# Optimization experiments

Measured on AMD Instinct MI355X. Metric: run time of the kernel, lower is better.

Reference implementation:

```python
import jax, jax.numpy as jnp
import numpy as np

L, S, M, N, E, H = 1024, 1024, 256, 8, 512, 8


def embed_rotary(x, cos, sin):
    # x: [B, T, E]; interleaved rotate-half as in RotaryPositionEncoding.embed_rotary
    x2 = jnp.stack([-x[..., 1::2], x[..., 0::2]], axis=-1).reshape(x.shape)
    return x * cos + x2 * sin


def setup_inputs() -> dict:
    key = jax.random.key(0)
    ks = jax.random.split(key, 12)
    return {
        "query": jax.random.normal(ks[0], (L, N, E), jnp.float32),
        "key": jax.random.normal(ks[1], (S, N, E), jnp.float32),
        "value": jax.random.normal(ks[2], (S, N, E), jnp.float32),
        "in_proj_weight": jax.random.normal(ks[3], (3 * E, E), jnp.float32) / np.sqrt(E).astype(np.float32),
        "in_proj_bias": jnp.zeros((3 * E,), jnp.float32),
        "out_proj_weight": jax.random.normal(ks[4], (E, E), jnp.float32) / np.sqrt(E).astype(np.float32),
        "out_proj_bias": jnp.zeros((E,), jnp.float32),
        "rot_q": jax.random.normal(ks[5], (N, L, E, 2), jnp.float32),
        "rot_k": jax.random.normal(ks[6], (N, S, E, 2), jnp.float32),
        "k_mem": jax.random.normal(ks[7], (M, N, E), jnp.float32),
        "v_mem": jax.random.normal(ks[8], (M, N, E), jnp.float32),
        "gate_attn": jax.random.normal(ks[9], (H,), jnp.float32),
        "mem_mask": jax.random.randint(ks[10], (N, M), 0, 2).astype(bool),
        "num_heads": H,
    }


def reference(query, key, value, in_proj_weight, in_proj_bias, out_proj_weight,
              out_proj_bias, rot_q, rot_k, k_mem, v_mem, gate_attn, mem_mask, num_heads):
    L_, N_, E_ = query.shape
    S_ = key.shape[0]
    H_ = num_heads
    hd = E_ // H_
    scale = float(hd) ** -0.5
    # separate q/k/v projections (qkv not identical path)
    q = query @ in_proj_weight[:E_].T + in_proj_bias[:E_]
    k = key @ in_proj_weight[E_:2 * E_].T + in_proj_bias[E_:2 * E_]
    v = value @ in_proj_weight[2 * E_:].T + in_proj_bias[2 * E_:]
    q = q * scale
    # inline rotary PE (applied in batch-first layout, then back)
    q = embed_rotary(q.transpose(1, 0, 2), rot_q[..., 0], rot_q[..., 1]).transpose(1, 0, 2)
    k = embed_rotary(k.transpose(1, 0, 2), rot_k[..., 0], rot_k[..., 1]).transpose(1, 0, 2)
    qh = q.reshape(L_, N_, H_, hd).transpose(1, 2, 0, 3)  # [N,H,L,hd]
    kh = k.reshape(S_, N_, H_, hd).transpose(1, 2, 0, 3)  # [N,H,S,hd]
    vh = v.reshape(S_, N_, H_, hd).transpose(1, 2, 0, 3)
    scores = jnp.einsum('nhld,nhsd->nhls', qh, kh)
    # slot-competition: softmax over queries (slots), then renormalize over keys
    w = jax.nn.softmax(scores, axis=2) + 1e-8
    w = w / w.sum(axis=-1, keepdims=True)
    attn = jnp.einsum('nhls,nhsd->nhld', w, vh)
    # memorizing-transformer style memory K/V branch with sigmoid head gating
    Mm = k_mem.shape[0]
    km = k_mem.reshape(Mm, N_, H_, hd).transpose(1, 2, 0, 3)  # [N,H,M,hd]
    vm = v_mem.reshape(Mm, N_, H_, hd).transpose(1, 2, 0, 3)
    sm = jnp.einsum('nhld,nhmd->nhlm', qh, km)
    sm = jnp.where(mem_mask[:, None, None, :], -1e9, sm)  # additive -inf mask
    wm = jax.nn.softmax(sm, axis=-1)
    om = jnp.einsum('nhlm,nhmd->nhld', wm, vm)
    gate = jax.nn.sigmoid(gate_attn)[None, :, None, None]  # [1,H,1,1]
    attn = gate * om + (1.0 - gate) * attn
    out = attn.transpose(2, 0, 1, 3).reshape(L_, N_, E_)  # back to [L,N,E]
    return out @ out_proj_weight.T + out_proj_bias
```

## Files before the change

### kernel.cpp

```cpp
#include <hip/hip_runtime.h>
#include <hip/hip_bf16.h>

typedef __hip_bfloat16 bf16;
typedef __bf16 bf16x8 __attribute__((ext_vector_type(8)));
typedef float f32x4 __attribute__((ext_vector_type(4)));

#define LQ 1024
#define SK 1024
#define MMEM 256
#define NB 8
#define EE 512
#define NH 8
#define HD 64
#define NBH 64

__device__ inline __bf16 tobf(float f) {
  __hip_bfloat16 h = __float2bfloat16(f);
  return *reinterpret_cast<__bf16*>(&h);
}
__device__ inline float bf2f(__bf16 x) {
  unsigned short u; __builtin_memcpy(&u, &x, 2);
  unsigned int v = (unsigned int)u << 16;
  float f; __builtin_memcpy(&f, &v, 4);
  return f;
}
__device__ inline f32x4 MFMA(bf16x8 a, bf16x8 b, f32x4 c) {
  return __builtin_amdgcn_mfma_f32_16x16x32_bf16(a, b, c, 0, 0, 0);
}

__device__ inline void gload_lds16(const bf16* g, void* l) {
  __builtin_amdgcn_global_load_lds(
      (const __attribute__((address_space(1))) void*)g,
      (__attribute__((address_space(3))) void*)l, 16, 0, 0);
}

__device__ inline bf16x8 load8(const float* p) {
  float4 a = *(const float4*)p;
  float4 b = *(const float4*)(p + 4);
  bf16x8 r;
  r[0] = tobf(a.x); r[1] = tobf(a.y); r[2] = tobf(a.z); r[3] = tobf(a.w);
  r[4] = tobf(b.x); r[5] = tobf(b.y); r[6] = tobf(b.z); r[7] = tobf(b.w);
  return r;
}

#define CVT_T0 524288
#define CVT_T3 98304
#define CVT_T4 32768
__global__ __launch_bounds__(256) void convert5(
    const float* __restrict__ q, const float* __restrict__ k,
    const float* __restrict__ v, const float* __restrict__ w,
    const float* __restrict__ o, bf16* __restrict__ qc, bf16* __restrict__ kc,
    bf16* __restrict__ vc, bf16* __restrict__ wc, bf16* __restrict__ oc)
{
  long long t = (long long)blockIdx.x * 256 + threadIdx.x;
  const float* src; bf16* dst; long long idx;
  if (t < CVT_T0)               { src = q; dst = qc; idx = t; }
  else if (t < 2 * CVT_T0)      { src = k; dst = kc; idx = t - CVT_T0; }
  else if (t < 3 * CVT_T0)      { src = v; dst = vc; idx = t - 2 * CVT_T0; }
  else if (t < 3 * CVT_T0 + CVT_T3) { src = w; dst = wc; idx = t - 3 * CVT_T0; }
  else                          { src = o; dst = oc; idx = t - 3 * CVT_T0 - CVT_T3; }
  *(bf16x8*)(dst + idx * 8) = load8(src + idx * 8);
}

__global__ __launch_bounds__(256) void gemm_proj3(
    const bf16* __restrict__ qc, const bf16* __restrict__ kc,
    const bf16* __restrict__ vc, const bf16* __restrict__ ipwb,
    const float* __restrict__ ipb, bf16* __restrict__ pq,
    bf16* __restrict__ pk, bf16* __restrict__ v_raw)
{
  __shared__ __align__(16) char smem[33792];
  __bf16* As = (__bf16*)smem;
  __bf16* Bs = (__bf16*)(smem + 16384);
  const int z = blockIdx.z;
  const bf16* A = (z == 0) ? qc : (z == 1) ? kc : vc;
  const bf16* W = ipwb + (long long)z * EE * EE;
  const float* bias = ipb + z * EE;
  const float alpha = (z == 0) ? 0.125f : 1.f;
  const int bid2 = blockIdx.y * gridDim.x + blockIdx.x;
  const int xcd = bid2 & 7, sub = bid2 >> 3;
  const int by = (xcd << 3) + (sub >> 2);
  const int bx = sub & 3;
  const int tm0 = by << 7, tn0 = bx << 7;
  const int t = threadIdx.x;
  const int wave = t >> 6, lane = t & 63;
  const int wrow0 = (wave & 1) << 6, wcol0 = (wave >> 1) << 6;
  const int m16 = lane & 15, quad = lane >> 4;

  const f32x4 zero = {0.f, 0.f, 0.f, 0.f};
  f32x4 acc[4][4];
#pragma unroll
  for (int mi = 0; mi < 4; ++mi)
#pragma unroll
    for (int ni = 0; ni < 4; ++ni) acc[mi][ni] = zero;

  const bf16* Ab = A + (long long)tm0 * EE;
  const bf16* Bb = W + (long long)tn0 * EE;
  const int ob_u = wave << 10;

  for (int k0 = 0; k0 < EE; k0 += 64) {
#pragma unroll
    for (int c = 0; c < 4; ++c) {
      int ob = (c << 12) + ob_u;
      int obl = ob + (lane << 4);
      int row = obl >> 7;
      int ce = (obl & 127) >> 1;
      gload_lds16(Ab + (long long)row * EE + k0 + ce, smem + ob);
      gload_lds16(Bb + (long long)row * EE + k0 + ce, smem + 16384 + ob);
    }
    __syncthreads();
#pragma unroll
    for (int kh = 0; kh < 2; ++kh) {
      bf16x8 av[4], bv[4];
#pragma unroll
      for (int i = 0; i < 4; ++i) {
        av[i] = *(bf16x8*)(As + ((wrow0 + (i << 4) + m16) << 6) + (kh << 5) + (quad << 3));
        bv[i] = *(bf16x8*)(Bs + ((wcol0 + (i << 4) + m16) << 6) + (kh << 5) + (quad << 3));
      }
#pragma unroll
      for (int mi = 0; mi < 4; ++mi)
#pragma unroll
        for (int ni = 0; ni < 4; ++ni)
          acc[mi][ni] = MFMA(av[mi], bv[ni], acc[mi][ni]);
    }
    __syncthreads();
  }

  __bf16 (*Cs)[132] = (__bf16(*)[132])smem;
#pragma unroll
  for (int mi = 0; mi < 4; ++mi)
#pragma unroll
    for (int ni = 0; ni < 4; ++ni) {
      int col = wcol0 + (ni << 4) + m16;
      float bv = bias[tn0 + col];
#pragma unroll
      for (int r = 0; r < 4; ++r)
        Cs[wrow0 + (mi << 4) + (quad << 2) + r][col] =
            tobf((acc[mi][ni][r] + bv) * alpha);
    }
  __syncthreads();
  bf16* O = (z == 0) ? pq : (z == 1) ? pk : v_raw;
  const int crow = t >> 1, ch0 = (t & 1) << 6;
  long long gb = (long long)(tm0 + crow) * EE + tn0 + ch0;
#pragma unroll
  for (int j = 0; j < 64; j += 8)
    *(uint4*)(O + gb + j) = *(uint4*)&Cs[crow][ch0 + j];
}

__global__ __launch_bounds__(256) void rotary_kernel(
    const bf16* __restrict__ pq, const bf16* __restrict__ pk,
    const float* __restrict__ rot_q, const float* __restrict__ rot_k,
    bf16* __restrict__ Qh, bf16* __restrict__ Kh)
{
  const bf16* src = blockIdx.y ? pk : pq;
  const float* rot = blockIdx.y ? rot_k : rot_q;
  bf16* dst = blockIdx.y ? Kh : Qh;
  const int t = threadIdx.x;
  const int row = (blockIdx.x << 2) + (t >> 6);
  const int e0 = (t & 63) << 3;
  const int l = row >> 3, n = row & 7;
  bf16x8 x = *(const bf16x8*)(src + (long long)row * EE + e0);
  const float* rp = rot + ((((long long)n * LQ + l) * EE + e0) << 1);
  __bf16 vals[8];
#pragma unroll
  for (int j = 0; j < 8; j += 2) {
    float4 cs4 = *(const float4*)(rp + (j << 1));
    float x0 = bf2f(x[j]);
    float x1 = bf2f(x[j + 1]);
    vals[j]     = tobf(x0 * cs4.x - x1 * cs4.y);
    vals[j + 1] = tobf(x1 * cs4.z + x0 * cs4.w);
  }
  const int h = e0 >> 6, d0 = e0 & 63;
  *(uint4*)(dst + (((long long)(n * NH + h) * LQ + l) * HD + d0)) = *(uint4*)vals;
}

__global__ __launch_bounds__(256) void colsum_kernel(
    const bf16* __restrict__ Qh, const bf16* __restrict__ Kh,
    float* __restrict__ csum)
{
  __shared__ __align__(16) __bf16 Ks[64][72];
  __shared__ __align__(16) __bf16 Qs[64][72];
  __shared__ float cpart[64][2];
  const int bid = blockIdx.y * gridDim.x + blockIdx.x;
  const int xcd = bid & 7, sub = bid >> 3;
  const int b = (xcd << 3) + (sub >> 4);
  const int st0 = (sub & 15) << 6;
  const int t = threadIdx.x;
  const int lrow = t >> 2, lcol = (t & 3) << 4;
  const int wave = t >> 6, lane = t & 63;
  const int wm = (wave & 1) << 5, wn = (wave >> 1) << 5;
  const int m16 = lane & 15, quad = lane >> 4;

  {
    const bf16* kp = Kh + ((long long)b * SK + st0 + lrow) * HD + lcol;
    *(bf16x8*)&Ks[lrow][lcol] = *(const bf16x8*)kp;
    *(bf16x8*)&Ks[lrow][lcol + 8] = *(const bf16x8*)(kp + 8);
  }
  __syncthreads();
  bf16x8 bk[2][2];
#pragma unroll
  for (int ni = 0; ni < 2; ++ni)
#pragma unroll
    for (int kh = 0; kh < 2; ++kh)
      bk[ni][kh] = *(bf16x8*)&Ks[wn + (ni << 4) + m16][(kh << 5) + (quad << 3)];
  __syncthreads();

  const f32x4 zero = {0.f, 0.f, 0.f, 0.f};
  float colp[2] = {0.f, 0.f};
  const bf16* qbase = Qh + ((long long)b * LQ + lrow) * HD + lcol;
  bf16x8 qr0 = *(const bf16x8*)qbase;
  bf16x8 qr1 = *(const bf16x8*)(qbase + 8);
  for (int lt = 0; lt < 16; ++lt) {
    *(bf16x8*)&Qs[lrow][lcol] = qr0;
    *(bf16x8*)&Qs[lrow][lcol + 8] = qr1;
    __syncthreads();
    if (lt < 15) {
      const bf16* qp = qbase + (long long)((lt + 1) << 6) * HD;
      qr0 = *(const bf16x8*)qp;
      qr1 = *(const bf16x8*)(qp + 8);
    }
    f32x4 s00 = zero, s01 = zero, s10 = zero, s11 = zero;
#pragma unroll
    for (int kh = 0; kh < 2; ++kh) {
      bf16x8 a0 = *(bf16x8*)&Qs[wm + m16][(kh << 5) + (quad << 3)];
      bf16x8 a1 = *(bf16x8*)&Qs[wm + 16 + m16][(kh << 5) + (quad << 3)];
      s00 = MFMA(a0, bk[0][kh], s00);
      s01 = MFMA(a0, bk[1][kh], s01);
      s10 = MFMA(a1, bk[0][kh], s10);
      s11 = MFMA(a1, bk[1][kh], s11);
    }
    f32x4 sacc[2][2] = {{s00, s01}, {s10, s11}};
#pragma unroll
    for (int mi = 0; mi < 2; ++mi)
#pragma unroll
      for (int ni = 0; ni < 2; ++ni)
#pragma unroll
        for (int r = 0; r < 4; ++r)
          colp[ni] += __expf(sacc[mi][ni][r]);
    __syncthreads();
  }
  for (int ni = 0; ni < 2; ++ni) {
    float v = colp[ni];
    v += __shfl_down(v, 32, 64);
    v += __shfl_down(v, 16, 64);
    if (quad == 0) cpart[wn + (ni << 4) + m16][wm >> 5] = v;
  }
  __syncthreads();
  if (t < 64) csum[b * SK + st0 + t] = cpart[t][0] + cpart[t][1];
}

__global__ __launch_bounds__(256) void vsum_kernel(
    const bf16* __restrict__ Vt, float* __restrict__ Vsum)
{
  int wid = blockIdx.x * 4 + (threadIdx.x >> 6);
  int lane = threadIdx.x & 63;
  const bf16* p = Vt + (long long)wid * SK + lane * 16;
  float s = 0.f;
  bf16x8 v0 = *(const bf16x8*)p;
  bf16x8 v1 = *(const bf16x8*)(p + 8);
#pragma unroll
  for (int j = 0; j < 8; ++j) s += bf2f(v0[j]) + bf2f(v1[j]);
  for (int off = 32; off; off >>= 1) s += __shfl_down(s, off, 64);
  if (lane == 0) Vsum[wid] = s;
}

__global__ __launch_bounds__(256) void attn_fused(
    const bf16* __restrict__ Qh, const bf16* __restrict__ Kh,
    const bf16* __restrict__ Vt, const bf16* __restrict__ km,
    const bf16* __restrict__ vmt, const float* __restrict__ csum,
    const float* __restrict__ Vsum, const int* __restrict__ mask,
    const float* __restrict__ gate, bf16* __restrict__ comb)
{
  __shared__ __align__(16) __bf16 Ks[64][72];
  __shared__ __align__(16) __bf16 Vs[64][72];
  __shared__ __align__(16) __bf16 Ps[4096];
  __shared__ __align__(16) float rcs[SK];
  __shared__ __align__(16) float mskf[MMEM];
  __shared__ float rpa[64][2];
  __shared__ float rpm[64][2];
  const int bid = blockIdx.y * gridDim.x + blockIdx.x;
  const int xcd = bid & 7, sub = bid >> 3;
  const int b = (xcd << 3) + (sub >> 4);
  const int tm0 = (sub & 15) << 6;
  const int n = b >> 3, h = b & 7;
  const int t = threadIdx.x;
  const int lrow = t >> 2, lcol = (t & 3) << 4;
  const int wave = t >> 6, lane = t & 63;
  const int wm = (wave & 1) << 5, wn = (wave >> 1) << 5;
  const int m16 = lane & 15, quad = lane >> 4;
  const int swz = (m16 & 7) << 4;

#pragma unroll
  for (int i = 0; i < 4; ++i)
    rcs[t + i * 256] = 1.f / csum[b * SK + t + i * 256];
  mskf[t] = mask[n * MMEM + t] ? 0.f : 1.f;
  {
    const bf16* qp = Qh + ((long long)b * LQ + tm0 + lrow) * HD + lcol;
    *(bf16x8*)&Ks[lrow][lcol] = *(const bf16x8*)qp;
    *(bf16x8*)&Ks[lrow][lcol + 8] = *(const bf16x8*)(qp + 8);
  }
  __syncthreads();
  bf16x8 aq[2][2];
#pragma unroll
  for (int li = 0; li < 2; ++li)
#pragma unroll
    for (int kh = 0; kh < 2; ++kh)
      aq[li][kh] = *(bf16x8*)&Ks[wm + (li << 4) + m16][(kh << 5) + (quad << 3)];
  __syncthreads();

  const f32x4 zero = {0.f, 0.f, 0.f, 0.f};
  f32x4 m00 = zero, m01 = zero, m10 = zero, m11 = zero;
  float rsm[2] = {0.f, 0.f};
  {
    const bf16* kbase = km + ((long long)b * MMEM + lrow) * HD + lcol;
    const bf16* vbase = vmt + ((long long)b * HD + lrow) * MMEM + lcol;
    bf16x8 kr0 = *(const bf16x8*)kbase;
    bf16x8 kr1 = *(const bf16x8*)(kbase + 8);
    bf16x8 vr0 = *(const bf16x8*)vbase;
    bf16x8 vr1 = *(const bf16x8*)(vbase + 8);
    for (int mt = 0; mt < 4; ++mt) {
      *(bf16x8*)&Ks[lrow][lcol] = kr0;
      *(bf16x8*)&Ks[lrow][lcol + 8] = kr1;
      *(bf16x8*)&Vs[lrow][lcol] = vr0;
      *(bf16x8*)&Vs[lrow][lcol + 8] = vr1;
      __syncthreads();
      if (mt < 3) {
        const bf16* kp = kbase + (long long)((mt + 1) << 6) * HD;
        const bf16* vp = vbase + ((mt + 1) << 6);
        kr0 = *(const bf16x8*)kp;
        kr1 = *(const bf16x8*)(kp + 8);
        vr0 = *(const bf16x8*)vp;
        vr1 = *(const bf16x8*)(vp + 8);
      }
      f32x4 s00 = zero, s01 = zero, s10 = zero, s11 = zero;
      __builtin_amdgcn_s_setprio(1);
#pragma unroll
      for (int kh = 0; kh < 2; ++kh) {
        bf16x8 ak0 = *(bf16x8*)&Ks[wn + m16][(kh << 5) + (quad << 3)];
        bf16x8 ak1 = *(bf16x8*)&Ks[wn + 16 + m16][(kh << 5) + (quad << 3)];
        s00 = MFMA(ak0, aq[0][kh], s00);
        s01 = MFMA(ak0, aq[1][kh], s01);
        s10 = MFMA(ak1, aq[0][kh], s10);
        s11 = MFMA(ak1, aq[1][kh], s11);
      }
      __builtin_amdgcn_s_setprio(0);
      {
        char* pA = (char*)Ps + (wm + m16) * 128;
        char* pB = (char*)Ps + (wm + 16 + m16) * 128;
#pragma unroll
        for (int si = 0; si < 2; ++si) {
          int sloc = wn + (si << 4) + (quad << 2);
          f32x4 mf4 = *(const f32x4*)&mskf[(mt << 6) + sloc];
          f32x4 sA = si ? s10 : s00;
          f32x4 sB = si ? s11 : s01;
          __bf16 vA[4], vB[4];
#pragma unroll
          for (int r = 0; r < 4; ++r) {
            float pa = __expf(sA[r]) * mf4[r];
            rsm[0] += pa; vA[r] = tobf(pa);
            float pb = __expf(sB[r]) * mf4[r];
            rsm[1] += pb; vB[r] = tobf(pb);
          }
          int sbyte = (sloc << 1) ^ swz;
          *(uint2*)(pA + sbyte) = *(uint2*)vA;
          *(uint2*)(pB + sbyte) = *(uint2*)vB;
        }
      }
      __syncthreads();
      __builtin_amdgcn_s_setprio(1);
#pragma unroll
      for (int kh = 0; kh < 2; ++kh) {
        int sb = (kh << 6) + (quad << 4);
        bf16x8 ap0 = *(bf16x8*)((char*)Ps + (wm + m16) * 128 + (sb ^ swz));
        bf16x8 ap1 = *(bf16x8*)((char*)Ps + (wm + 16 + m16) * 128 + (sb ^ swz));
        bf16x8 bv0 = *(bf16x8*)&Vs[wn + m16][(kh << 5) + (quad << 3)];
        bf16x8 bv1 = *(bf16x8*)&Vs[wn + 16 + m16][(kh << 5) + (quad << 3)];
        m00 = MFMA(ap0, bv0, m00);
        m01 = MFMA(ap0, bv1, m01);
        m10 = MFMA(ap1, bv0, m10);
        m11 = MFMA(ap1, bv1, m11);
      }
      __builtin_amdgcn_s_setprio(0);
      __syncthreads();
    }
  }

  f32x4 o00 = zero, o01 = zero, o10 = zero, o11 = zero;
  float rsa[2] = {0.f, 0.f};
  {
    const bf16* kbase = Kh + ((long long)b * SK + lrow) * HD + lcol;
    const bf16* vbase = Vt + ((long long)b * HD + lrow) * SK + lcol;
    bf16x8 kr0 = *(const bf16x8*)kbase;
    bf16x8 kr1 = *(const bf16x8*)(kbase + 8);
    bf16x8 vr0 = *(const bf16x8*)vbase;
    bf16x8 vr1 = *(const bf16x8*)(vbase + 8);
    for (int st = 0; st < 16; ++st) {
      *(bf16x8*)&Ks[lrow][lcol] = kr0;
      *(bf16x8*)&Ks[lrow][lcol + 8] = kr1;
      *(bf16x8*)&Vs[lrow][lcol] = vr0;
      *(bf16x8*)&Vs[lrow][lcol + 8] = vr1;
      __syncthreads();
      if (st < 15) {
        const bf16* kp = kbase + (long long)((st + 1) << 6) * HD;
        const bf16* vp = vbase + ((st + 1) << 6);
        kr0 = *(const bf16x8*)kp;
        kr1 = *(const bf16x8*)(kp + 8);
        vr0 = *(const bf16x8*)vp;
        vr1 = *(const bf16x8*)(vp + 8);
      }
      f32x4 s00 = zero, s01 = zero, s10 = zero, s11 = zero;
      __builtin_amdgcn_s_setprio(1);
#pragma unroll
      for (int kh = 0; kh < 2; ++kh) {
        bf16x8 ak0 = *(bf16x8*)&Ks[wn + m16][(kh << 5) + (quad << 3)];
        bf16x8 ak1 = *(bf16x8*)&Ks[wn + 16 + m16][(kh << 5) + (quad << 3)];
        s00 = MFMA(ak0, aq[0][kh], s00);
        s01 = MFMA(ak0, aq[1][kh], s01);
        s10 = MFMA(ak1, aq[0][kh], s10);
        s11 = MFMA(ak1, aq[1][kh], s11);
      }
      __builtin_amdgcn_s_setprio(0);
      {
        char* pA = (char*)Ps + (wm + m16) * 128;
        char* pB = (char*)Ps + (wm + 16 + m16) * 128;
#pragma unroll
        for (int si = 0; si < 2; ++si) {
          int sloc = wn + (si << 4) + (quad << 2);
          f32x4 rc4 = *(const f32x4*)&rcs[(st << 6) + sloc];
          f32x4 sA = si ? s10 : s00;
          f32x4 sB = si ? s11 : s01;
          __bf16 vA[4], vB[4];
#pragma unroll
          for (int r = 0; r < 4; ++r) {
            float pa = __expf(sA[r]) * rc4[r];
            rsa[0] += pa; vA[r] = tobf(pa);
            float pb = __expf(sB[r]) * rc4[r];
            rsa[1] += pb; vB[r] = tobf(pb);
          }
          int sbyte = (sloc << 1) ^ swz;
          *(uint2*)(pA + sbyte) = *(uint2*)vA;
          *(uint2*)(pB + sbyte) = *(uint2*)vB;
        }
      }
      __syncthreads();
      __builtin_amdgcn_s_setprio(1);
#pragma unroll
      for (int kh = 0; kh < 2; ++kh) {
        int sb = (kh << 6) + (quad << 4);
        bf16x8 ap0 = *(bf16x8*)((char*)Ps + (wm + m16) * 128 + (sb ^ swz));
        bf16x8 ap1 = *(bf16x8*)((char*)Ps + (wm + 16 + m16) * 128 + (sb ^ swz));
        bf16x8 bv0 = *(bf16x8*)&Vs[wn + m16][(kh << 5) + (quad << 3)];
        bf16x8 bv1 = *(bf16x8*)&Vs[wn + 16 + m16][(kh << 5) + (quad << 3)];
        o00 = MFMA(ap0, bv0, o00);
        o01 = MFMA(ap0, bv1, o01);
        o10 = MFMA(ap1, bv0, o10);
        o11 = MFMA(ap1, bv1, o11);
      }
      __builtin_amdgcn_s_setprio(0);
      __syncthreads();
    }
  }

#pragma unroll
  for (int li = 0; li < 2; ++li) {
    float va = rsa[li];
    va += __shfl_xor(va, 16, 64);
    va += __shfl_xor(va, 32, 64);
    float vm = rsm[li];
    vm += __shfl_xor(vm, 16, 64);
    vm += __shfl_xor(vm, 32, 64);
    if (quad == 0) {
      rpa[wm + (li << 4) + m16][wn >> 5] = va;
      rpm[wm + (li << 4) + m16][wn >> 5] = vm;
    }
  }
  __syncthreads();

  const float* vs = Vsum + b * HD;
  const float g = 1.f / (1.f + __expf(-gate[h]));
  f32x4 oacc[2][2] = {{o00, o01}, {o10, o11}};
  f32x4 macc[2][2] = {{m00, m01}, {m10, m11}};
  for (int mi = 0; mi < 2; ++mi)
    for (int ni = 0; ni < 2; ++ni) {
      int col = wn + (ni << 4) + m16;
      float vsc = 1e-8f * vs[col];
      for (int r = 0; r < 4; ++r) {
        int row = wm + (mi << 4) + (quad << 2) + r;
        float ra = rpa[row][0] + rpa[row][1];
        float rm = rpm[row][0] + rpm[row][1];
        float oa = (oacc[mi][ni][r] + vsc) / (ra + (float)SK * 1e-8f);
        float om = macc[mi][ni][r] / rm;
        Ks[row][col] = tobf(g * om + (1.f - g) * oa);
      }
    }
  __syncthreads();
  uint4 u0 = *(uint4*)&Ks[lrow][lcol];
  uint4 u1 = *(uint4*)&Ks[lrow][lcol + 8];
  long long gb = ((long long)b * LQ + tm0 + lrow) * HD + lcol;
  *(uint4*)(comb + gb) = u0;
  *(uint4*)(comb + gb + 8) = u1;
}

__global__ __launch_bounds__(256) void gemm_out(
    const bf16* __restrict__ comb, const bf16* __restrict__ opwb,
    const float* __restrict__ opb, float* __restrict__ out)
{
  __shared__ __align__(16) char smem[32768];
  __bf16* As = (__bf16*)smem;
  __bf16* Bs = (__bf16*)(smem + 16384);
  const int bid2 = blockIdx.y * gridDim.x + blockIdx.x;
  const int xcd = bid2 & 7, sub = bid2 >> 3;
  const int by = (xcd << 3) + (sub >> 2);
  const int bx = sub & 3;
  const int tm0 = by << 7, tn0 = bx << 7;
  const int t = threadIdx.x;
  const int wave = t >> 6, lane = t & 63;
  const int wrow0 = (wave & 1) << 6, wcol0 = (wave >> 1) << 6;
  const int m16 = lane & 15, quad = lane >> 4;

  const f32x4 zero = {0.f, 0.f, 0.f, 0.f};
  f32x4 acc[4][4];
#pragma unroll
  for (int mi = 0; mi < 4; ++mi)
#pragma unroll
    for (int ni = 0; ni < 4; ++ni) acc[mi][ni] = zero;

  const bf16* Bb = opwb + (long long)tn0 * EE;
  const int ob_u = wave << 10;

  for (int k0 = 0; k0 < EE; k0 += 64) {
    const int h = k0 >> 6;
#pragma unroll
    for (int c = 0; c < 4; ++c) {
      int ob = (c << 12) + ob_u;
      int obl = ob + (lane << 4);
      int row = obl >> 7;
      int ce = (obl & 127) >> 1;
      int arow = tm0 + row;
      int l = arow >> 3, nn = arow & 7;
      gload_lds16(comb + (((long long)(nn * NH + h) * LQ + l) * HD + ce),
                  smem + ob);
      gload_lds16(Bb + (long long)row * EE + k0 + ce, smem + 16384 + ob);
    }
    __syncthreads();
#pragma unroll
    for (int kh = 0; kh < 2; ++kh) {
      bf16x8 av[4], bv[4];
#pragma unroll
      for (int i = 0; i < 4; ++i) {
        av[i] = *(bf16x8*)(As + ((wrow0 + (i << 4) + m16) << 6) + (kh << 5) + (quad << 3));
        bv[i] = *(bf16x8*)(Bs + ((wcol0 + (i << 4) + m16) << 6) + (kh << 5) + (quad << 3));
      }
#pragma unroll
      for (int mi = 0; mi < 4; ++mi)
#pragma unroll
        for (int ni = 0; ni < 4; ++ni)
          acc[mi][ni] = MFMA(av[mi], bv[ni], acc[mi][ni]);
    }
    __syncthreads();
  }

#pragma unroll
  for (int mi = 0; mi < 4; ++mi)
#pragma unroll
    for (int ni = 0; ni < 4; ++ni) {
      int col = tn0 + wcol0 + (ni << 4) + m16;
      float bv = opb[col];
      int row0 = tm0 + wrow0 + (mi << 4) + (quad << 2);
#pragma unroll
      for (int r = 0; r < 4; ++r)
        out[(long long)(row0 + r) * EE + col] = acc[mi][ni][r] + bv;
    }
}

__global__ __launch_bounds__(256) void v_transpose(
    const bf16* __restrict__ raw, bf16* __restrict__ Vt)
{
  __shared__ __align__(16) __bf16 Ts[64][72];
  const int bh = blockIdx.y;
  const int n = bh >> 3, h = bh & 7;
  const int s0 = blockIdx.x << 6;
  const int t = threadIdx.x;
  const int i = t >> 2, c0 = (t & 3) << 4;
  const bf16* rp = raw + ((long long)(s0 + i) * NB + n) * EE + h * HD + c0;
  *(bf16x8*)&Ts[i][c0] = *(const bf16x8*)rp;
  *(bf16x8*)&Ts[i][c0 + 8] = *(const bf16x8*)(rp + 8);
  __syncthreads();
  const int d = t >> 2, j0 = (t & 3) << 4;
  __bf16 vals[16];
#pragma unroll
  for (int j = 0; j < 16; ++j) vals[j] = Ts[j0 + j][d];
  bf16* wp = Vt + ((long long)bh * HD + d) * SK + s0 + j0;
  *(uint4*)wp = *(uint4*)&vals[0];
  *(uint4*)(wp + 8) = *(uint4*)&vals[8];
}

__global__ __launch_bounds__(256) void mem_prep(
    const float* __restrict__ k_mem, const float* __restrict__ v_mem,
    bf16* __restrict__ km, bf16* __restrict__ vmt)
{
  __shared__ __align__(16) __bf16 Ts[64][72];
  const int bh = blockIdx.y;
  const int n = bh >> 3, h = bh & 7;
  const int m0 = blockIdx.x << 6;
  const int t = threadIdx.x;
  const int i = t >> 2, c0 = (t & 3) << 4;
  const float* kp = k_mem + ((long long)(m0 + i) * NB + n) * EE + h * HD + c0;
  const float* vp = v_mem + ((long long)(m0 + i) * NB + n) * EE + h * HD + c0;
  bf16x8 kv0 = load8(kp), kv1 = load8(kp + 8);
  bf16x8 vv0 = load8(vp), vv1 = load8(vp + 8);
  bf16* kw = km + ((long long)bh * MMEM + m0 + i) * HD + c0;
  *(bf16x8*)kw = kv0;
  *(bf16x8*)(kw + 8) = kv1;
  *(bf16x8*)&Ts[i][c0] = vv0;
  *(bf16x8*)&Ts[i][c0 + 8] = vv1;
  __syncthreads();
  const int d = t >> 2, j0 = (t & 3) << 4;
  __bf16 vals[16];
#pragma unroll
  for (int j = 0; j < 16; ++j) vals[j] = Ts[j0 + j][d];
  bf16* wp = vmt + ((long long)bh * HD + d) * MMEM + m0 + j0;
  *(uint4*)wp = *(uint4*)&vals[0];
  *(uint4*)(wp + 8) = *(uint4*)&vals[8];
}

extern "C" void kernel_launch(void* const* d_in, const int* in_sizes, int n_in,
                              void* d_out, int out_size, void* d_ws, size_t ws_size,
                              hipStream_t stream) {
  const float* query = (const float*)d_in[0];
  const float* key   = (const float*)d_in[1];
  const float* value = (const float*)d_in[2];
  const float* ipw   = (const float*)d_in[3];
  const float* ipb   = (const float*)d_in[4];
  const float* opw   = (const float*)d_in[5];
  const float* opb   = (const float*)d_in[6];
  const float* rot_q = (const float*)d_in[7];
  const float* rot_k = (const float*)d_in[8];
  const float* k_mem = (const float*)d_in[9];
  const float* v_mem = (const float*)d_in[10];
  const float* gate  = (const float*)d_in[11];
  const int*  mask   = (const int*)d_in[12];
  float* out = (float*)d_out;

  char* w = (char*)d_ws;
  size_t off = 0;
  auto carve = [&](size_t bytes) -> char* {
    char* p = w + off;
    off += (bytes + 255) & ~(size_t)255;
    return p;
  };
  bf16* qc    = (bf16*)carve((size_t)LQ * NB * EE * 2);
  bf16* kc    = (bf16*)carve((size_t)SK * NB * EE * 2);
  bf16* vc    = (bf16*)carve((size_t)SK * NB * EE * 2);
  bf16* ipwb  = (bf16*)carve((size_t)3 * EE * EE * 2);
  bf16* opwb  = (bf16*)carve((size_t)EE * EE * 2);
  bf16* v_raw = (bf16*)carve((size_t)SK * NB * EE * 2);
  bf16* Qh    = (bf16*)carve((size_t)NBH * LQ * HD * 2);
  bf16* Kh    = (bf16*)carve((size_t)NBH * SK * HD * 2);
  bf16* Vt    = (bf16*)carve((size_t)NBH * HD * SK * 2);
  bf16* km    = (bf16*)carve((size_t)NBH * MMEM * HD * 2);
  bf16* vmt   = (bf16*)carve((size_t)NBH * HD * MMEM * 2);
  float* csum = (float*)carve((size_t)NBH * SK * 4);
  float* Vsum = (float*)carve((size_t)NBH * HD * 4);
  bf16* comb  = (bf16*)carve((size_t)NBH * LQ * HD * 2);
  bf16* pkbuf = (bf16*)carve((size_t)NBH * LQ * HD * 2);
  if (off > ws_size) {
    hipMemsetAsync(d_out, 0, (size_t)out_size * 4, stream);
    return;
  }
  bf16* pq = comb;
  bf16* pk = pkbuf;

  convert5<<<(3 * CVT_T0 + CVT_T3 + CVT_T4) / 256, 256, 0, stream>>>(
      query, key, value, ipw, opw, qc, kc, vc, ipwb, opwb);

  gemm_proj3<<<dim3(EE / 128, (LQ * NB) / 128, 3), 256, 0, stream>>>(
      qc, kc, vc, ipwb, ipb, pq, pk, v_raw);

  rotary_kernel<<<dim3((LQ * NB) / 4, 2), 256, 0, stream>>>(
      pq, pk, rot_q, rot_k, Qh, Kh);

  v_transpose<<<dim3(SK / 64, NBH), 256, 0, stream>>>(v_raw, Vt);
  vsum_kernel<<<(NBH * HD) / 4, 256, 0, stream>>>(Vt, Vsum);
  mem_prep<<<dim3(MMEM / 64, NBH), 256, 0, stream>>>(k_mem, v_mem, km, vmt);

  colsum_kernel<<<dim3(SK / 64, NBH), 256, 0, stream>>>(Qh, Kh, csum);

  attn_fused<<<dim3(LQ / 64, NBH), 256, 0, stream>>>(
      Qh, Kh, Vt, km, vmt, csum, Vsum, mask, gate, comb);

  gemm_out<<<dim3(4, 64), 256, 0, stream>>>(comb, opwb, opb, out);
}
```

Measured before the change: 304.9 us.

## Double-buffer K/V/Q tiles via direct global-to-LDS loads and fuse V column sums

Colsum and attention kernels now stream K/V/Q tiles straight into swizzled, double-buffered LDS with direct global-to-LDS loads, prefetching the next tile while the current one is computed. The memory and main attention loops share one pipeline, so the first main tile is prefetched during the last memory tile. The colsum kernel covers 128 keys per block, halving Q rereads. The separate vsum kernel is folded into v_transpose with shuffles and atomics, which needs a memset beforehand. The cost is more LDS and atomic ordering nondeterminism in Vsum.

```diff
diff --git a/kernel.cpp b/kernel.cpp
--- a/kernel.cpp
+++ b/kernel.cpp
@@ -177,90 +177,100 @@
     const bf16* __restrict__ Qh, const bf16* __restrict__ Kh,
     float* __restrict__ csum)
 {
-  __shared__ __align__(16) __bf16 Ks[64][72];
-  __shared__ __align__(16) __bf16 Qs[64][72];
-  __shared__ float cpart[64][2];
+  __shared__ __align__(16) char QdB[16384];
+  __shared__ float cpart[128][2];
   const int bid = blockIdx.y * gridDim.x + blockIdx.x;
   const int xcd = bid & 7, sub = bid >> 3;
-  const int b = (xcd << 3) + (sub >> 4);
-  const int st0 = (sub & 15) << 6;
+  const int b = (xcd << 3) + (sub >> 3);
+  const int st0 = (sub & 7) << 7;
   const int t = threadIdx.x;
-  const int lrow = t >> 2, lcol = (t & 3) << 4;
   const int wave = t >> 6, lane = t & 63;
   const int wm = (wave & 1) << 5, wn = (wave >> 1) << 5;
   const int m16 = lane & 15, quad = lane >> 4;
-
-  {
-    const bf16* kp = Kh + ((long long)b * SK + st0 + lrow) * HD + lcol;
-    *(bf16x8*)&Ks[lrow][lcol] = *(const bf16x8*)kp;
-    *(bf16x8*)&Ks[lrow][lcol + 8] = *(const bf16x8*)(kp + 8);
-  }
+  const int swz = (m16 & 7) << 4;
+
+  bf16x8 bk[2][2][2];
+#pragma unroll
+  for (int g = 0; g < 2; ++g)
+#pragma unroll
+    for (int ni = 0; ni < 2; ++ni)
+#pragma unroll
+      for (int kh = 0; kh < 2; ++kh)
+        bk[g][ni][kh] = *(const bf16x8*)(
+            Kh + ((long long)b * SK + st0 + (g << 6) + wn + (ni << 4) + m16) * HD
+               + (kh << 5) + (quad << 3));
+
+  int ldsoff[2]; const bf16* qsrc[2];
+#pragma unroll
+  for (int c = 0; c < 2; ++c) {
+    int tb = (wave << 11) + (c << 10) + (lane << 4);
+    int row = tb >> 7, cb = tb & 127;
+    int srcb = cb ^ ((row & 7) << 4);
+    ldsoff[c] = (wave << 11) + (c << 10);
+    qsrc[c] = Qh + ((long long)b * LQ + row) * HD + (srcb >> 1);
+  }
+#pragma unroll
+  for (int c = 0; c < 2; ++c) gload_lds16(qsrc[c], QdB + ldsoff[c]);
   __syncthreads();
-  bf16x8 bk[2][2];
-#pragma unroll
-  for (int ni = 0; ni < 2; ++ni)
-#pragma unroll
-    for (int kh = 0; kh < 2; ++kh)
-      bk[ni][kh] = *(bf16x8*)&Ks[wn + (ni << 4) + m16][(kh << 5) + (quad << 3)];
+
+  const f32x4 zero = {0.f, 0.f, 0.f, 0.f};
+  float colp[2][2] = {{0.f, 0.f}, {0.f, 0.f}};
+  int cur = 0;
+  for (int lt = 0; lt < 16; ++lt) {
+    if (lt < 15) {
+#pragma unroll
+      for (int c = 0; c < 2; ++c)
+        gload_lds16(qsrc[c] + (long long)(lt + 1) * 64 * HD,
+                    QdB + ((cur ^ 1) << 13) + ldsoff[c]);
+    }
+    bf16x8 a0k[2], a1k[2];
+#pragma unroll
+    for (int kh = 0; kh < 2; ++kh) {
+      int byt = ((kh << 6) + (quad << 4)) ^ swz;
+      a0k[kh] = *(bf16x8*)(QdB + (cur << 13) + (wm + m16) * 128 + byt);
+      a1k[kh] = *(bf16x8*)(QdB + (cur << 13) + (wm + 16 + m16) * 128 + byt);
+    }
+    f32x4 s[2][2][2];
+#pragma unroll
+    for (int g = 0; g < 2; ++g)
+#pragma unroll
+      for (int mi = 0; mi < 2; ++mi)
+#pragma unroll
+        for (int ni = 0; ni < 2; ++ni) s[g][mi][ni] = zero;
+    __builtin_amdgcn_s_setprio(1);
+#pragma unroll
+    for (int g = 0; g < 2; ++g)
+#pragma unroll
+      for (int kh = 0; kh < 2; ++kh) {
+        s[g][0][0] = MFMA(a0k[kh], bk[g][0][kh], s[g][0][0]);
+        s[g][0][1] = MFMA(a0k[kh], bk[g][1][kh], s[g][0][1]);
+        s[g][1][0] = MFMA(a1k[kh], bk[g][0][kh], s[g][1][0]);
+        s[g][1][1] = MFMA(a1k[kh], bk[g][1][kh], s[g][1][1]);
+      }
+    __builtin_amdgcn_s_setprio(0);
+#pragma unroll
+    for (int g = 0; g < 2; ++g)
+#pragma unroll
+      for (int mi = 0; mi < 2; ++mi)
+#pragma unroll
+        for (int ni = 0; ni < 2; ++ni)
+#pragma unroll
+          for (int r = 0; r < 4; ++r)
+            colp[g][ni] += __expf(s[g][mi][ni][r]);
+    __syncthreads();
+    cur ^= 1;
+  }
+#pragma unroll
+  for (int g = 0; g < 2; ++g)
+#pragma unroll
+    for (int ni = 0; ni < 2; ++ni) {
+      float v = colp[g][ni];
+      v += __shfl_down(v, 32, 64);
+      v += __shfl_down(v, 16, 64);
+      if (quad == 0) cpart[(g << 6) + wn + (ni << 4) + m16][wm >> 5] = v;
+    }
   __syncthreads();
-
-  const f32x4 zero = {0.f, 0.f, 0.f, 0.f};
-  float colp[2] = {0.f, 0.f};
-  const bf16* qbase = Qh + ((long long)b * LQ + lrow) * HD + lcol;
-  bf16x8 qr0 = *(const bf16x8*)qbase;
-  bf16x8 qr1 = *(const bf16x8*)(qbase + 8);
-  for (int lt = 0; lt < 16; ++lt) {
-    *(bf16x8*)&Qs[lrow][lcol] = qr0;
-    *(bf16x8*)&Qs[lrow][lcol + 8] = qr1;
-    __syncthreads();
-    if (lt < 15) {
-      const bf16* qp = qbase + (long long)((lt + 1) << 6) * HD;
-      qr0 = *(const bf16x8*)qp;
-      qr1 = *(const bf16x8*)(qp + 8);
-    }
-    f32x4 s00 = zero, s01 = zero, s10 = zero, s11 = zero;
-#pragma unroll
-    for (int kh = 0; kh < 2; ++kh) {
-      bf16x8 a0 = *(bf16x8*)&Qs[wm + m16][(kh << 5) + (quad << 3)];
-      bf16x8 a1 = *(bf16x8*)&Qs[wm + 16 + m16][(kh << 5) + (quad << 3)];
-      s00 = MFMA(a0, bk[0][kh], s00);
-      s01 = MFMA(a0, bk[1][kh], s01);
-      s10 = MFMA(a1, bk[0][kh], s10);
-      s11 = MFMA(a1, bk[1][kh], s11);
-    }
-    f32x4 sacc[2][2] = {{s00, s01}, {s10, s11}};
-#pragma unroll
-    for (int mi = 0; mi < 2; ++mi)
-#pragma unroll
-      for (int ni = 0; ni < 2; ++ni)
-#pragma unroll
-        for (int r = 0; r < 4; ++r)
-          colp[ni] += __expf(sacc[mi][ni][r]);
-    __syncthreads();
-  }
-  for (int ni = 0; ni < 2; ++ni) {
-    float v = colp[ni];
-    v += __shfl_down(v, 32, 64);
-    v += __shfl_down(v, 16, 64);
-    if (quad == 0) cpart[wn + (ni << 4) + m16][wm >> 5] = v;
-  }
-  __syncthreads();
-  if (t < 64) csum[b * SK + st0 + t] = cpart[t][0] + cpart[t][1];
-}
-
-__global__ __launch_bounds__(256) void vsum_kernel(
-    const bf16* __restrict__ Vt, float* __restrict__ Vsum)
-{
-  int wid = blockIdx.x * 4 + (threadIdx.x >> 6);
-  int lane = threadIdx.x & 63;
-  const bf16* p = Vt + (long long)wid * SK + lane * 16;
-  float s = 0.f;
-  bf16x8 v0 = *(const bf16x8*)p;
-  bf16x8 v1 = *(const bf16x8*)(p + 8);
-#pragma unroll
-  for (int j = 0; j < 8; ++j) s += bf2f(v0[j]) + bf2f(v1[j]);
-  for (int off = 32; off; off >>= 1) s += __shfl_down(s, off, 64);
-  if (lane == 0) Vsum[wid] = s;
+  if (t < 128) csum[b * SK + st0 + t] = cpart[t][0] + cpart[t][1];
 }
 
 __global__ __launch_bounds__(256) void attn_fused(
@@ -270,9 +280,9 @@
     const float* __restrict__ Vsum, const int* __restrict__ mask,
     const float* __restrict__ gate, bf16* __restrict__ comb)
 {
-  __shared__ __align__(16) __bf16 Ks[64][72];
-  __shared__ __align__(16) __bf16 Vs[64][72];
-  __shared__ __align__(16) __bf16 Ps[4096];
+  __shared__ __align__(16) char KdB[16384];
+  __shared__ __align__(16) char VdB[16384];
+  __shared__ __align__(16) char PsB[8192];
   __shared__ __align__(16) float rcs[SK];
   __shared__ __align__(16) float mskf[MMEM];
   __shared__ float rpa[64][2];
@@ -293,171 +303,180 @@
   for (int i = 0; i < 4; ++i)
     rcs[t + i * 256] = 1.f / csum[b * SK + t + i * 256];
   mskf[t] = mask[n * MMEM + t] ? 0.f : 1.f;
-  {
-    const bf16* qp = Qh + ((long long)b * LQ + tm0 + lrow) * HD + lcol;
-    *(bf16x8*)&Ks[lrow][lcol] = *(const bf16x8*)qp;
-    *(bf16x8*)&Ks[lrow][lcol + 8] = *(const bf16x8*)(qp + 8);
-  }
-  __syncthreads();
+
   bf16x8 aq[2][2];
 #pragma unroll
   for (int li = 0; li < 2; ++li)
 #pragma unroll
     for (int kh = 0; kh < 2; ++kh)
-      aq[li][kh] = *(bf16x8*)&Ks[wm + (li << 4) + m16][(kh << 5) + (quad << 3)];
+      aq[li][kh] = *(const bf16x8*)(
+          Qh + ((long long)b * LQ + tm0 + wm + (li << 4) + m16) * HD
+             + (kh << 5) + (quad << 3));
+
+  int ldsoff[2]; int srow[2], scol[2];
+#pragma unroll
+  for (int c = 0; c < 2; ++c) {
+    int tb = (wave << 11) + (c << 10) + (lane << 4);
+    int row = tb >> 7, cb = tb & 127;
+    int srcb = cb ^ ((row & 7) << 4);
+    ldsoff[c] = (wave << 11) + (c << 10);
+    srow[c] = row; scol[c] = srcb >> 1;
+  }
+  const bf16* kmain = Kh + (long long)b * SK * HD;
+  const bf16* vmain = Vt + (long long)b * HD * SK;
+  const bf16* kmem = km + (long long)b * MMEM * HD;
+  const bf16* vmem = vmt + (long long)b * HD * MMEM;
+
+#pragma unroll
+  for (int c = 0; c < 2; ++c) {
+    gload_lds16(kmem + (long long)srow[c] * HD + scol[c], KdB + ldsoff[c]);
+    gload_lds16(vmem + (long long)srow[c] * MMEM + scol[c], VdB + ldsoff[c]);
+  }
   __syncthreads();
 
   const f32x4 zero = {0.f, 0.f, 0.f, 0.f};
   f32x4 m00 = zero, m01 = zero, m10 = zero, m11 = zero;
+  f32x4 o00 = zero, o01 = zero, o10 = zero, o11 = zero;
   float rsm[2] = {0.f, 0.f};
-  {
-    const bf16* kbase = km + ((long long)b * MMEM + lrow) * HD + lcol;
-    const bf16* vbase = vmt + ((long long)b * HD + lrow) * MMEM + lcol;
-    bf16x8 kr0 = *(const bf16x8*)kbase;
-    bf16x8 kr1 = *(const bf16x8*)(kbase + 8);
-    bf16x8 vr0 = *(const bf16x8*)vbase;
-    bf16x8 vr1 = *(const bf16x8*)(vbase + 8);
-    for (int mt = 0; mt < 4; ++mt) {
-      *(bf16x8*)&Ks[lrow][lcol] = kr0;
-      *(bf16x8*)&Ks[lrow][lcol + 8] = kr1;
-      *(bf16x8*)&Vs[lrow][lcol] = vr0;
-      *(bf16x8*)&Vs[lrow][lcol + 8] = vr1;
-      __syncthreads();
-      if (mt < 3) {
-        const bf16* kp = kbase + (long long)((mt + 1) << 6) * HD;
-        const bf16* vp = vbase + ((mt + 1) << 6);
-        kr0 = *(const bf16x8*)kp;
-        kr1 = *(const bf16x8*)(kp + 8);
-        vr0 = *(const bf16x8*)vp;
-        vr1 = *(const bf16x8*)(vp + 8);
-      }
-      f32x4 s00 = zero, s01 = zero, s10 = zero, s11 = zero;
-      __builtin_amdgcn_s_setprio(1);
-#pragma unroll
-      for (int kh = 0; kh < 2; ++kh) {
-        bf16x8 ak0 = *(bf16x8*)&Ks[wn + m16][(kh << 5) + (quad << 3)];
-        bf16x8 ak1 = *(bf16x8*)&Ks[wn + 16 + m16][(kh << 5) + (quad << 3)];
-        s00 = MFMA(ak0, aq[0][kh], s00);
-        s01 = MFMA(ak0, aq[1][kh], s01);
-        s10 = MFMA(ak1, aq[0][kh], s10);
-        s11 = MFMA(ak1, aq[1][kh], s11);
-      }
-      __builtin_amdgcn_s_setprio(0);
-      {
-        char* pA = (char*)Ps + (wm + m16) * 128;
-        char* pB = (char*)Ps + (wm + 16 + m16) * 128;
-#pragma unroll
-        for (int si = 0; si < 2; ++si) {
-          int sloc = wn + (si << 4) + (quad << 2);
-          f32x4 mf4 = *(const f32x4*)&mskf[(mt << 6) + sloc];
-          f32x4 sA = si ? s10 : s00;
-          f32x4 sB = si ? s11 : s01;
-          __bf16 vA[4], vB[4];
-#pragma unroll
-          for (int r = 0; r < 4; ++r) {
-            float pa = __expf(sA[r]) * mf4[r];
-            rsm[0] += pa; vA[r] = tobf(pa);
-            float pb = __expf(sB[r]) * mf4[r];
-            rsm[1] += pb; vB[r] = tobf(pb);
-          }
-          int sbyte = (sloc << 1) ^ swz;
-          *(uint2*)(pA + sbyte) = *(uint2*)vA;
-          *(uint2*)(pB + sbyte) = *(uint2*)vB;
+  float rsa[2] = {0.f, 0.f};
+  int cur = 0;
+
+  for (int mt = 0; mt < 4; ++mt) {
+    if (mt < 3) {
+#pragma unroll
+      for (int c = 0; c < 2; ++c) {
+        gload_lds16(kmem + ((long long)((mt + 1) << 6) + srow[c]) * HD + scol[c],
+                    KdB + ((cur ^ 1) << 13) + ldsoff[c]);
+        gload_lds16(vmem + (long long)srow[c] * MMEM + ((mt + 1) << 6) + scol[c],
+                    VdB + ((cur ^ 1) << 13) + ldsoff[c]);
+      }
+    } else {
+#pragma unroll
+      for (int c = 0; c < 2; ++c) {
+        gload_lds16(kmain + (long long)srow[c] * HD + scol[c],
+                    KdB + ((cur ^ 1) << 13) + ldsoff[c]);
+        gload_lds16(vmain + (long long)srow[c] * SK + scol[c],
+                    VdB + ((cur ^ 1) << 13) + ldsoff[c]);
+      }
+    }
+    f32x4 s00 = zero, s01 = zero, s10 = zero, s11 = zero;
+    __builtin_amdgcn_s_setprio(1);
+#pragma unroll
+    for (int kh = 0; kh < 2; ++kh) {
+      int byt = ((kh << 6) + (quad << 4)) ^ swz;
+      bf16x8 ak0 = *(bf16x8*)(KdB + (cur << 13) + (wn + m16) * 128 + byt);
+      bf16x8 ak1 = *(bf16x8*)(KdB + (cur << 13) + (wn + 16 + m16) * 128 + byt);
+      s00 = MFMA(ak0, aq[0][kh], s00);
+      s01 = MFMA(ak0, aq[1][kh], s01);
+      s10 = MFMA(ak1, aq[0][kh], s10);
+      s11 = MFMA(ak1, aq[1][kh], s11);
+    }
+    __builtin_amdgcn_s_setprio(0);
+    {
+      char* pA = PsB + (wm + m16) * 128;
+      char* pB = PsB + (wm + 16 + m16) * 128;
+#pragma unroll
+      for (int si = 0; si < 2; ++si) {
+        int sloc = wn + (si << 4) + (quad << 2);
+        f32x4 mf4 = *(const f32x4*)&mskf[(mt << 6) + sloc];
+        f32x4 sA = si ? s10 : s00;
+        f32x4 sB = si ? s11 : s01;
+        __bf16 vA[4], vB[4];
+#pragma unroll
+        for (int r = 0; r < 4; ++r) {
+          float pa = __expf(sA[r]) * mf4[r];
+          rsm[0] += pa; vA[r] = tobf(pa);
+          float pb = __expf(sB[r]) * mf4[r];
+          rsm[1] += pb; vB[r] = tobf(pb);
         }
-      }
-      __syncthreads();
-      __builtin_amdgcn_s_setprio(1);
-#pragma unroll
-      for (int kh = 0; kh < 2; ++kh) {
-        int sb = (kh << 6) + (quad << 4);
-        bf16x8 ap0 = *(bf16x8*)((char*)Ps + (wm + m16) * 128 + (sb ^ swz));
-        bf16x8 ap1 = *(bf16x8*)((char*)Ps + (wm + 16 + m16) * 128 + (sb ^ swz));
-        bf16x8 bv0 = *(bf16x8*)&Vs[wn + m16][(kh << 5) + (quad << 3)];
-        bf16x8 bv1 = *(bf16x8*)&Vs[wn + 16 + m16][(kh << 5) + (quad << 3)];
-        m00 = MFMA(ap0, bv0, m00);
-        m01 = MFMA(ap0, bv1, m01);
-        m10 = MFMA(ap1, bv0, m10);
-        m11 = MFMA(ap1, bv1, m11);
-      }
-      __builtin_amdgcn_s_setprio(0);
-      __syncthreads();
-    }
-  }
-
-  f32x4 o00 = zero, o01 = zero, o10 = zero, o11 = zero;
-  float rsa[2] = {0.f, 0.f};
-  {
-    const bf16* kbase = Kh + ((long long)b * SK + lrow) * HD + lcol;
-    const bf16* vbase = Vt + ((long long)b * HD + lrow) * SK + lcol;
-    bf16x8 kr0 = *(const bf16x8*)kbase;
-    bf16x8 kr1 = *(const bf16x8*)(kbase + 8);
-    bf16x8 vr0 = *(const bf16x8*)vbase;
-    bf16x8 vr1 = *(const bf16x8*)(vbase + 8);
-    for (int st = 0; st < 16; ++st) {
-      *(bf16x8*)&Ks[lrow][lcol] = kr0;
-      *(bf16x8*)&Ks[lrow][lcol + 8] = kr1;
-      *(bf16x8*)&Vs[lrow][lcol] = vr0;
-      *(bf16x8*)&Vs[lrow][lcol + 8] = vr1;
-      __syncthreads();
-      if (st < 15) {
-        const bf16* kp = kbase + (long long)((st + 1) << 6) * HD;
-        const bf16* vp = vbase + ((st + 1) << 6);
-        kr0 = *(const bf16x8*)kp;
-        kr1 = *(const bf16x8*)(kp + 8);
-        vr0 = *(const bf16x8*)vp;
-        vr1 = *(const bf16x8*)(vp + 8);
-      }
-      f32x4 s00 = zero, s01 = zero, s10 = zero, s11 = zero;
-      __builtin_amdgcn_s_setprio(1);
-#pragma unroll
-      for (int kh = 0; kh < 2; ++kh) {
-        bf16x8 ak0 = *(bf16x8*)&Ks[wn + m16][(kh << 5) + (quad << 3)];
-        bf16x8 ak1 = *(bf16x8*)&Ks[wn + 16 + m16][(kh << 5) + (quad << 3)];
-        s00 = MFMA(ak0, aq[0][kh], s00);
-        s01 = MFMA(ak0, aq[1][kh], s01);
-        s10 = MFMA(ak1, aq[0][kh], s10);
-        s11 = MFMA(ak1, aq[1][kh], s11);
-      }
-      __builtin_amdgcn_s_setprio(0);
-      {
-        char* pA = (char*)Ps + (wm + m16) * 128;
-        char* pB = (char*)Ps + (wm + 16 + m16) * 128;
-#pragma unroll
-        for (int si = 0; si < 2; ++si) {
-          int sloc = wn + (si << 4) + (quad << 2);
-          f32x4 rc4 = *(const f32x4*)&rcs[(st << 6) + sloc];
-          f32x4 sA = si ? s10 : s00;
-          f32x4 sB = si ? s11 : s01;
-          __bf16 vA[4], vB[4];
-#pragma unroll
-          for (int r = 0; r < 4; ++r) {
-            float pa = __expf(sA[r]) * rc4[r];
-            rsa[0] += pa; vA[r] = tobf(pa);
-            float pb = __expf(sB[r]) * rc4[r];
-            rsa[1] += pb; vB[r] = tobf(pb);
-          }
-          int sbyte = (sloc << 1) ^ swz;
-          *(uint2*)(pA + sbyte) = *(uint2*)vA;
-          *(uint2*)(pB + sbyte) = *(uint2*)vB;
+        int sbyte = (sloc << 1) ^ swz;
+        *(uint2*)(pA + sbyte) = *(uint2*)vA;
+        *(uint2*)(pB + sbyte) = *(uint2*)vB;
+      }
+    }
+    __syncthreads();
+    __builtin_amdgcn_s_setprio(1);
+#pragma unroll
+    for (int kh = 0; kh < 2; ++kh) {
+      int sb = (kh << 6) + (quad << 4);
+      int byt = sb ^ swz;
+      bf16x8 ap0 = *(bf16x8*)(PsB + (wm + m16) * 128 + byt);
+      bf16x8 ap1 = *(bf16x8*)(PsB + (wm + 16 + m16) * 128 + byt);
+      bf16x8 bv0 = *(bf16x8*)(VdB + (cur << 13) + (wn + m16) * 128 + byt);
+      bf16x8 bv1 = *(bf16x8*)(VdB + (cur << 13) + (wn + 16 + m16) * 128 + byt);
+      m00 = MFMA(ap0, bv0, m00);
+      m01 = MFMA(ap0, bv1, m01);
+      m10 = MFMA(ap1, bv0, m10);
+      m11 = MFMA(ap1, bv1, m11);
+    }
+    __builtin_amdgcn_s_setprio(0);
+    __syncthreads();
+    cur ^= 1;
+  }
+
+  for (int st = 0; st < 16; ++st) {
+    if (st < 15) {
+#pragma unroll
+      for (int c = 0; c < 2; ++c) {
+        gload_lds16(kmain + ((long long)((st + 1) << 6) + srow[c]) * HD + scol[c],
+                    KdB + ((cur ^ 1) << 13) + ldsoff[c]);
+        gload_lds16(vmain + (long long)srow[c] * SK + ((st + 1) << 6) + scol[c],
+                    VdB + ((cur ^ 1) << 13) + ldsoff[c]);
+      }
+    }
+    f32x4 s00 = zero, s01 = zero, s10 = zero, s11 = zero;
+    __builtin_amdgcn_s_setprio(1);
+#pragma unroll
+    for (int kh = 0; kh < 2; ++kh) {
+      int byt = ((kh << 6) + (quad << 4)) ^ swz;
+      bf16x8 ak0 = *(bf16x8*)(KdB + (cur << 13) + (wn + m16) * 128 + byt);
+      bf16x8 ak1 = *(bf16x8*)(KdB + (cur << 13) + (wn + 16 + m16) * 128 + byt);
+      s00 = MFMA(ak0, aq[0][kh], s00);
+      s01 = MFMA(ak0, aq[1][kh], s01);
+      s10 = MFMA(ak1, aq[0][kh], s10);
+      s11 = MFMA(ak1, aq[1][kh], s11);
+    }
+    __builtin_amdgcn_s_setprio(0);
+    {
+      char* pA = PsB + (wm + m16) * 128;
+      char* pB = PsB + (wm + 16 + m16) * 128;
+#pragma unroll
+      for (int si = 0; si < 2; ++si) {
+        int sloc = wn + (si << 4) + (quad << 2);
+        f32x4 rc4 = *(const f32x4*)&rcs[(st << 6) + sloc];
+        f32x4 sA = si ? s10 : s00;
+        f32x4 sB = si ? s11 : s01;
+        __bf16 vA[4], vB[4];
+#pragma unroll
+        for (int r = 0; r < 4; ++r) {
+          float pa = __expf(sA[r]) * rc4[r];
+          rsa[0] += pa; vA[r] = tobf(pa);
+          float pb = __expf(sB[r]) * rc4[r];
+          rsa[1] += pb; vB[r] = tobf(pb);
         }
-      }
-      __syncthreads();
-      __builtin_amdgcn_s_setprio(1);
-#pragma unroll
-      for (int kh = 0; kh < 2; ++kh) {
-        int sb = (kh << 6) + (quad << 4);
-        bf16x8 ap0 = *(bf16x8*)((char*)Ps + (wm + m16) * 128 + (sb ^ swz));
-        bf16x8 ap1 = *(bf16x8*)((char*)Ps + (wm + 16 + m16) * 128 + (sb ^ swz));
-        bf16x8 bv0 = *(bf16x8*)&Vs[wn + m16][(kh << 5) + (quad << 3)];
-        bf16x8 bv1 = *(bf16x8*)&Vs[wn + 16 + m16][(kh << 5) + (quad << 3)];
-        o00 = MFMA(ap0, bv0, o00);
-        o01 = MFMA(ap0, bv1, o01);
-        o10 = MFMA(ap1, bv0, o10);
-        o11 = MFMA(ap1, bv1, o11);
-      }
-      __builtin_amdgcn_s_setprio(0);
-      __syncthreads();
-    }
+        int sbyte = (sloc << 1) ^ swz;
+        *(uint2*)(pA + sbyte) = *(uint2*)vA;
+        *(uint2*)(pB + sbyte) = *(uint2*)vB;
+      }
+    }
+    __syncthreads();
+    __builtin_amdgcn_s_setprio(1);
+#pragma unroll
+    for (int kh = 0; kh < 2; ++kh) {
+      int sb = (kh << 6) + (quad << 4);
+      int byt = sb ^ swz;
+      bf16x8 ap0 = *(bf16x8*)(PsB + (wm + m16) * 128 + byt);
+      bf16x8 ap1 = *(bf16x8*)(PsB + (wm + 16 + m16) * 128 + byt);
+      bf16x8 bv0 = *(bf16x8*)(VdB + (cur << 13) + (wn + m16) * 128 + byt);
+      bf16x8 bv1 = *(bf16x8*)(VdB + (cur << 13) + (wn + 16 + m16) * 128 + byt);
+      o00 = MFMA(ap0, bv0, o00);
+      o01 = MFMA(ap0, bv1, o01);
+      o10 = MFMA(ap1, bv0, o10);
+      o11 = MFMA(ap1, bv1, o11);
+    }
+    __builtin_amdgcn_s_setprio(0);
+    __syncthreads();
+    cur ^= 1;
   }
 
 #pragma unroll
@@ -489,12 +508,13 @@
         float rm = rpm[row][0] + rpm[row][1];
         float oa = (oacc[mi][ni][r] + vsc) / (ra + (float)SK * 1e-8f);
         float om = macc[mi][ni][r] / rm;
-        Ks[row][col] = tobf(g * om + (1.f - g) * oa);
+        *(__bf16*)(PsB + row * 128 + (((col << 1) ^ ((row & 7) << 4)))) =
+            tobf(g * om + (1.f - g) * oa);
       }
     }
   __syncthreads();
-  uint4 u0 = *(uint4*)&Ks[lrow][lcol];
-  uint4 u1 = *(uint4*)&Ks[lrow][lcol + 8];
+  uint4 u0 = *(uint4*)(PsB + lrow * 128 + (((lcol << 1)) ^ ((lrow & 7) << 4)));
+  uint4 u1 = *(uint4*)(PsB + lrow * 128 + ((((lcol + 8) << 1)) ^ ((lrow & 7) << 4)));
   long long gb = ((long long)b * LQ + tm0 + lrow) * HD + lcol;
   *(uint4*)(comb + gb) = u0;
   *(uint4*)(comb + gb + 8) = u1;
@@ -573,7 +593,8 @@
 }
 
 __global__ __launch_bounds__(256) void v_transpose(
-    const bf16* __restrict__ raw, bf16* __restrict__ Vt)
+    const bf16* __restrict__ raw, bf16* __restrict__ Vt,
+    float* __restrict__ Vsum)
 {
   __shared__ __align__(16) __bf16 Ts[64][72];
   const int bh = blockIdx.y;
@@ -587,11 +608,15 @@
   __syncthreads();
   const int d = t >> 2, j0 = (t & 3) << 4;
   __bf16 vals[16];
-#pragma unroll
-  for (int j = 0; j < 16; ++j) vals[j] = Ts[j0 + j][d];
+  float part = 0.f;
+#pragma unroll
+  for (int j = 0; j < 16; ++j) { vals[j] = Ts[j0 + j][d]; part += bf2f(vals[j]); }
   bf16* wp = Vt + ((long long)bh * HD + d) * SK + s0 + j0;
   *(uint4*)wp = *(uint4*)&vals[0];
   *(uint4*)(wp + 8) = *(uint4*)&vals[8];
+  part += __shfl_xor(part, 1, 64);
+  part += __shfl_xor(part, 2, 64);
+  if ((t & 3) == 0) atomicAdd(&Vsum[bh * HD + d], part);
 }
 
 __global__ __launch_bounds__(256) void mem_prep(
@@ -672,6 +697,7 @@
 
   convert5<<<(3 * CVT_T0 + CVT_T3 + CVT_T4) / 256, 256, 0, stream>>>(
       query, key, value, ipw, opw, qc, kc, vc, ipwb, opwb);
+  hipMemsetAsync(Vsum, 0, (size_t)NBH * HD * 4, stream);
 
   gemm_proj3<<<dim3(EE / 128, (LQ * NB) / 128, 3), 256, 0, stream>>>(
       qc, kc, vc, ipwb, ipb, pq, pk, v_raw);
@@ -679,11 +705,10 @@
   rotary_kernel<<<dim3((LQ * NB) / 4, 2), 256, 0, stream>>>(
       pq, pk, rot_q, rot_k, Qh, Kh);
 
-  v_transpose<<<dim3(SK / 64, NBH), 256, 0, stream>>>(v_raw, Vt);
-  vsum_kernel<<<(NBH * HD) / 4, 256, 0, stream>>>(Vt, Vsum);
+  v_transpose<<<dim3(SK / 64, NBH), 256, 0, stream>>>(v_raw, Vt, Vsum);
   mem_prep<<<dim3(MMEM / 64, NBH), 256, 0, stream>>>(k_mem, v_mem, km, vmt);
 
-  colsum_kernel<<<dim3(SK / 64, NBH), 256, 0, stream>>>(Qh, Kh, csum);
+  colsum_kernel<<<dim3(SK / 128, NBH), 256, 0, stream>>>(Qh, Kh, csum);
 
   attn_fused<<<dim3(LQ / 64, NBH), 256, 0, stream>>>(
       Qh, Kh, Vt, km, vmt, csum, Vsum, mask, gate, comb);
```

After: 305.2 us. Within noise of the previous version (+0.1%).
